# Kernel optimization log

Measured on AMD Instinct MI355X. Metric: run time of the kernel, lower is better.

The kernel has to match this reference:

```python
import jax, jax.numpy as jnp
import numpy as np

K_HOPS = 3
ALPHA = 0.3
DELTA = 0.5
KL_EPS = 1e-10
BN_EPS = 1e-5
DEG_MIN = 1e-6

B, T, N, F_IN, H, T_OUT = 8, 12, 1536, 1, 64, 12
HID2 = 2 * H  # MLP hidden width = 128


def setup_inputs() -> dict:
    key = jax.random.key(0)
    ks = jax.random.split(key, 20)
    s = 0.05
    TH = T * H
    inp = {
        "x": jax.random.normal(ks[0], (B, T, N, F_IN), jnp.float32),
        # AdaptiveBiDiffConv weights (stored as (in, out))
        "W1": jax.random.normal(ks[1], (F_IN, H), jnp.float32) * s,
        "W2": jax.random.normal(ks[2], (F_IN, H), jnp.float32) * s,
        # encoder MLPBlock: Linear(TH,128) ReLU Linear(128,128) ReLU Linear(128,64) + proj(TH,64), BN(64)
        "enc_w1": jax.random.normal(ks[3], (TH, HID2), jnp.float32) * s,
        "enc_b1": jnp.zeros((HID2,), jnp.float32),
        "enc_w2": jax.random.normal(ks[4], (HID2, HID2), jnp.float32) * s,
        "enc_b2": jnp.zeros((HID2,), jnp.float32),
        "enc_w3": jax.random.normal(ks[5], (HID2, H), jnp.float32) * s,
        "enc_b3": jnp.zeros((H,), jnp.float32),
        "enc_proj": jax.random.normal(ks[6], (TH, H), jnp.float32) * s,
        "enc_bn_g": jnp.ones((H,), jnp.float32),
        "enc_bn_b": jnp.zeros((H,), jnp.float32),
        "enc_bn_m": jnp.zeros((H,), jnp.float32),
        "enc_bn_v": jnp.ones((H,), jnp.float32),
        # decoder MLPBlock: Linear(64,128) ReLU Linear(128,128) ReLU Linear(128,12) + proj(64,12), BN(12)
        "dec_w1": jax.random.normal(ks[7], (H, HID2), jnp.float32) * s,
        "dec_b1": jnp.zeros((HID2,), jnp.float32),
        "dec_w2": jax.random.normal(ks[8], (HID2, HID2), jnp.float32) * s,
        "dec_b2": jnp.zeros((HID2,), jnp.float32),
        "dec_w3": jax.random.normal(ks[9], (HID2, T_OUT), jnp.float32) * s,
        "dec_b3": jnp.zeros((T_OUT,), jnp.float32),
        "dec_proj": jax.random.normal(ks[10], (H, T_OUT), jnp.float32) * s,
        "dec_bn_g": jnp.ones((T_OUT,), jnp.float32),
        "dec_bn_b": jnp.zeros((T_OUT,), jnp.float32),
        "dec_bn_m": jnp.zeros((T_OUT,), jnp.float32),
        "dec_bn_v": jnp.ones((T_OUT,), jnp.float32),
    }
    return inp


def _row_norm(A):
    return A / jnp.maximum(A.sum(-1, keepdims=True), DEG_MIN)


def _mlp_block(z, w1, b1, w2, b2, w3, b3, proj, g, be, m, v):
    h = jax.nn.relu(z @ w1 + b1)
    h = jax.nn.relu(h @ w2 + b2)
    o = (h @ w3 + b3) + z @ proj
    # BatchNorm1d, eval mode over last (channel) axis
    return (o - m) / jnp.sqrt(v + BN_EPS) * g + be


def _forward(x, W1, W2,
             enc_w1, enc_b1, enc_w2, enc_b2, enc_w3, enc_b3, enc_proj,
             enc_bn_g, enc_bn_b, enc_bn_m, enc_bn_v,
             dec_w1, dec_b1, dec_w2, dec_b2, dec_w3, dec_b3, dec_proj,
             dec_bn_g, dec_bn_b, dec_bn_m, dec_bn_v):
    b, t, n, _ = x.shape
    # ---- KL adjacency (fused form: avoids (B,N,N,T) broadcast) ----
    p = jax.nn.softmax(jnp.transpose(x[..., 0], (0, 2, 1)), axis=-1)  # (B,N,T)
    logp = jnp.log(p + KL_EPS)
    # kl[b,i,j] = sum_t p_i (logp_i - logp_j)
    kl = jnp.sum(p * logp, axis=-1, keepdims=True) - jnp.einsum('bit,bjt->bij', p, logp)
    A = (kl < DELTA).astype(x.dtype)  # (B,N,N)
    A_fwd = _row_norm(A)
    A_bwd = _row_norm(jnp.swapaxes(A, -1, -2))
    # ---- bidirectional diffusion conv (x_k never updated in original loop) ----
    x_flow = x[..., :1]                    # (B,T,N,1)
    x_res = x_flow @ W1                    # (B,T,N,H)
    xw = x_flow @ W2                       # (B,T,N,H)
    fwd = jnp.einsum('bij,btjh->btih', A_fwd, xw)
    bwd = jnp.einsum('bij,btjh->btih', A_bwd, xw)
    x_p = jax.nn.relu(x_res + K_HOPS * (ALPHA * fwd + (1.0 - ALPHA) * bwd))
    # ---- temporal MLP encoder/decoder ----
    x_flat = jnp.transpose(x_p, (0, 2, 1, 3)).reshape(b, n, t * x_p.shape[-1])  # (B,N,T*H)
    x_e = _mlp_block(x_flat, enc_w1, enc_b1, enc_w2, enc_b2, enc_w3, enc_b3,
                     enc_proj, enc_bn_g, enc_bn_b, enc_bn_m, enc_bn_v)  # (B,N,H)
    x_d = _mlp_block(x_e, dec_w1, dec_b1, dec_w2, dec_b2, dec_w3, dec_b3,
                     dec_proj, dec_bn_g, dec_bn_b, dec_bn_m, dec_bn_v)  # (B,N,T_out)
    return jnp.transpose(x_d, (0, 2, 1))[..., None]  # (B,T_out,N,1)


def reference(x, W1, W2,
              enc_w1, enc_b1, enc_w2, enc_b2, enc_w3, enc_b3, enc_proj,
              enc_bn_g, enc_bn_b, enc_bn_m, enc_bn_v,
              dec_w1, dec_b1, dec_w2, dec_b2, dec_w3, dec_b3, dec_proj,
              dec_bn_g, dec_bn_b, dec_bn_m, dec_bn_v):
    return _forward(x, W1, W2,
                    enc_w1, enc_b1, enc_w2, enc_b2, enc_w3, enc_b3, enc_proj,
                    enc_bn_g, enc_bn_b, enc_bn_m, enc_bn_v,
                    dec_w1, dec_b1, dec_w2, dec_b2, dec_w3, dec_b3, dec_proj,
                    dec_bn_g, dec_bn_b, dec_bn_m, dec_bn_v)
```

## Files before the change

kernel.cpp:

```cpp
#include <hip/hip_runtime.h>
#include <hip/hip_bf16.h>


namespace {

constexpr int Bn = 8, Nn = 1536, TOUT = 12;
constexpr int Mrows = Bn * Nn;
constexpr int JS = 8;

typedef __attribute__((ext_vector_type(8))) short bf8;
typedef __attribute__((ext_vector_type(4))) float f4;
typedef unsigned short ush;

__device__ __forceinline__ float b2f(__hip_bfloat16 v) { return __bfloat162float(v); }
__device__ __forceinline__ ush f2bu(float f) {
  union { __hip_bfloat16 h; ush u; } c; c.h = __float2bfloat16(f); return c.u;
}
__device__ __forceinline__ float bu2f(ush u) {
  union { unsigned int i; float f; } c; c.i = ((unsigned)u) << 16; return c.f;
}
__device__ __forceinline__ float ldraw(const void* p, size_t i, int fl) {
  return fl ? ((const float*)p)[i] : b2f(((const __hip_bfloat16*)p)[i]);
}

struct SmallTab { const void* src[16]; int n[16]; int off[16]; };

__global__ __launch_bounds__(256) void detect_small(
    const void* __restrict__ x, int* __restrict__ flag, SmallTab st,
    float* __restrict__ CS) {
  __shared__ int cnt; __shared__ int fls;
  if (threadIdx.x == 0) cnt = 0;
  __syncthreads();
  const ush* u = (const ush*)x;
  int c = 0;
#pragma unroll
  for (int s = 0; s < 16; ++s) {
    ush v = u[threadIdx.x + s * 256];
    if (((v >> 7) & 0xFF) >= 140) c++;
  }
  atomicAdd(&cnt, c);
  __syncthreads();
  if (threadIdx.x == 0) { fls = (cnt > 64) ? 1 : 0; flag[0] = fls; }
  __syncthreads();
  int fl = fls;
  for (int i = 0; i < 16; ++i)
    for (int e = threadIdx.x; e < st.n[i]; e += 256)
      CS[st.off[i] + e] = ldraw(st.src[i], e, fl);
}

__global__ __launch_bounds__(256) void prep_kernel(
    const void* __restrict__ xraw, const int* __restrict__ flag,
    float* __restrict__ xT, float* __restrict__ sd,
    ush* __restrict__ pA, ush* __restrict__ lA,
    ush* __restrict__ phi16, ush* __restrict__ plo16,
    ush* __restrict__ lhi16, ush* __restrict__ llo16,
    ush* __restrict__ Xc) {
  int tid = blockIdx.x * 256 + threadIdx.x;
  if (tid >= Mrows) return;
  int b = tid / Nn, n = tid - b * Nn;
  int fl = flag[0];
  float xv[12];
#pragma unroll
  for (int t = 0; t < 12; ++t)
    xv[t] = ldraw(xraw, (size_t)(b * 12 + t) * Nn + n, fl);
  float mx = xv[0];
#pragma unroll
  for (int t = 1; t < 12; ++t) mx = fmaxf(mx, xv[t]);
  float e[12], Z = 0.f;
#pragma unroll
  for (int t = 0; t < 12; ++t) { e[t] = expf(xv[t] - mx); Z += e[t]; }
  float invZ = 1.f / Z;
  float sacc = 0.f;
  ush pa[32], la[32], ph[16], pl[16], lh[16], ll[16];
#pragma unroll
  for (int k = 0; k < 32; ++k) { pa[k] = 0; la[k] = 0; }
#pragma unroll
  for (int k = 0; k < 16; ++k) { ph[k] = 0; pl[k] = 0; lh[k] = 0; ll[k] = 0; }
#pragma unroll
  for (int t = 0; t < 12; ++t) {
    float pv = e[t] * invZ;
    float lv = logf(pv + 1e-10f);
    sacc += pv * lv;
    xT[(size_t)tid * 12 + t] = xv[t];
    ush phv = f2bu(pv);  float plv = pv - bu2f(phv);
    ush lhv = f2bu(lv);  float llv = lv - bu2f(lhv);
    pa[t] = phv; pa[16 + t] = f2bu(plv);
    la[t] = lhv; la[16 + t] = f2bu(llv);
    ph[t] = phv; pl[t] = f2bu(plv);
    lh[t] = lhv; ll[t] = f2bu(llv);
    Xc[((size_t)(b * 16 + t)) * Nn + n] = f2bu(xv[t]);
  }
  Xc[((size_t)(b * 16 + 12)) * Nn + n] = 0x3F80;
#pragma unroll
  for (int t = 13; t < 16; ++t) Xc[((size_t)(b * 16 + t)) * Nn + n] = 0;
  sd[tid] = sacc;
  {
    uint4* d = (uint4*)(pA + (size_t)tid * 32);
    const uint4* s = (const uint4*)pa;
    d[0] = s[0]; d[1] = s[1]; d[2] = s[2]; d[3] = s[3];
    uint4* d2 = (uint4*)(lA + (size_t)tid * 32);
    const uint4* s2 = (const uint4*)la;
    d2[0] = s2[0]; d2[1] = s2[1]; d2[2] = s2[2]; d2[3] = s2[3];
    ((uint4*)(phi16 + (size_t)tid * 16))[0] = ((const uint4*)ph)[0];
    ((uint4*)(phi16 + (size_t)tid * 16))[1] = ((const uint4*)ph)[1];
    ((uint4*)(plo16 + (size_t)tid * 16))[0] = ((const uint4*)pl)[0];
    ((uint4*)(plo16 + (size_t)tid * 16))[1] = ((const uint4*)pl)[1];
    ((uint4*)(lhi16 + (size_t)tid * 16))[0] = ((const uint4*)lh)[0];
    ((uint4*)(lhi16 + (size_t)tid * 16))[1] = ((const uint4*)lh)[1];
    ((uint4*)(llo16 + (size_t)tid * 16))[0] = ((const uint4*)ll)[0];
    ((uint4*)(llo16 + (size_t)tid * 16))[1] = ((const uint4*)ll)[1];
  }
}

struct RepTab { const void* src[8]; int Nc[8]; int NCT[8]; int lb[9]; };

__global__ __launch_bounds__(256) void repack_kernel(
    RepTab tab, const int* __restrict__ flag, ush* __restrict__ Wf) {
  int idx = blockIdx.x * 256 + threadIdx.x;
  if (idx >= tab.lb[8]) return;
  int fl = flag[0];
  int mi = 0;
#pragma unroll
  for (int i = 1; i < 8; ++i) if (idx >= tab.lb[i]) mi = i;
  int li = idx - tab.lb[mi];
  int NCT = tab.NCT[mi], Nc = tab.Nc[mi];
  int per = NCT * 64;
  int c0 = li / per, rem = li - c0 * per;
  int ct = rem >> 6, l = rem & 63;
  int q = l >> 4, m = l & 15;
  int col = ct * 16 + m;
  ush* d = Wf + (size_t)idx * 8;
#pragma unroll
  for (int j = 0; j < 8; ++j) {
    int k = c0 * 32 + q * 8 + j;
    d[j] = (col < Nc) ? f2bu(ldraw(tab.src[mi], (size_t)k * Nc + col, fl)) : 0;
  }
}

__global__ __launch_bounds__(256) void kl_mfma(
    const ush* __restrict__ pA, const ush* __restrict__ lA,
    const ush* __restrict__ phi16, const ush* __restrict__ plo16,
    const ush* __restrict__ lhi16, const ush* __restrict__ llo16,
    const ush* __restrict__ Xc, const float* __restrict__ sd,
    float* __restrict__ psf, float* __restrict__ psb) {
  __shared__ ush T1[4][512], T2[4][512];
  int tid = threadIdx.x, w = tid >> 6, l = tid & 63, q = l >> 4, n = l & 15;
  int blk = blockIdx.x;
  int b = blk / 192, rem = blk % 192, ig = rem >> 3, js = rem & 7;
  int i0 = ig * 64 + w * 16;
  int rowb = b * Nn;

  if (q >= 2) {
    uint4 z4 = {0, 0, 0, 0};
    *(uint4*)(&T1[w][(size_t)l * 8]) = z4;
    *(uint4*)(&T2[w][(size_t)l * 8]) = z4;
  }

  bf8 z8 = {0, 0, 0, 0, 0, 0, 0, 0};
  bf8 aP = *(const bf8*)(pA + ((size_t)(rowb + i0 + n)) * 32 + q * 8);
  bf8 aL = *(const bf8*)(lA + ((size_t)(rowb + i0 + n)) * 32 + q * 8);
  bf8 aPh = (q < 2) ? aP : z8;
  bf8 aLh = (q < 2) ? aL : z8;
  float selfI[4];
#pragma unroll
  for (int r = 0; r < 4; ++r) selfI[r] = sd[rowb + i0 + q * 4 + r];

  f4 accF = {0.f, 0.f, 0.f, 0.f}, accB = {0.f, 0.f, 0.f, 0.f};

  for (int jt = 0; jt < 12; ++jt) {
    int jl = js * 192 + jt * 16;
    size_t bb = ((size_t)(rowb + jl + n)) * 16 + (q & 1) * 8;
    bf8 bLh = *(const bf8*)(lhi16 + bb);
    bf8 bLo = *(const bf8*)(llo16 + bb);
    bf8 bPh = *(const bf8*)(phi16 + bb);
    bf8 bPo = *(const bf8*)(plo16 + bb);
    float selfJ = sd[rowb + jl + n];

    f4 s1 = {0.f, 0.f, 0.f, 0.f}, s2 = {0.f, 0.f, 0.f, 0.f};
    s1 = __builtin_amdgcn_mfma_f32_16x16x32_bf16(aP, bLh, s1, 0, 0, 0);
    s1 = __builtin_amdgcn_mfma_f32_16x16x32_bf16(aPh, bLo, s1, 0, 0, 0);
    s2 = __builtin_amdgcn_mfma_f32_16x16x32_bf16(aL, bPh, s2, 0, 0, 0);
    s2 = __builtin_amdgcn_mfma_f32_16x16x32_bf16(aLh, bPo, s2, 0, 0, 0);

    int qk = n >> 3, kj = n & 7;
#pragma unroll
    for (int r = 0; r < 4; ++r) {
      int pos = (qk * 16 + q * 4 + r) * 8 + kj;
      T1[w][pos] = (selfI[r] - s1[r] < 0.5f) ? (ush)0x3F80 : (ush)0;
      T2[w][pos] = (selfJ - s2[r] < 0.5f) ? (ush)0x3F80 : (ush)0;
    }
    bf8 af1 = *(const bf8*)(&T1[w][(size_t)l * 8]);
    bf8 af2 = *(const bf8*)(&T2[w][(size_t)l * 8]);
    bf8 xf = (q < 2)
        ? *(const bf8*)(Xc + ((size_t)(b * 16 + n)) * Nn + jl + q * 8) : z8;
    accF = __builtin_amdgcn_mfma_f32_16x16x32_bf16(af1, xf, accF, 0, 0, 0);
    accB = __builtin_amdgcn_mfma_f32_16x16x32_bf16(af2, xf, accB, 0, 0, 0);
  }
#pragma unroll
  for (int r = 0; r < 4; ++r) {
    size_t o = ((size_t)js * Mrows + rowb + i0 + q * 4 + r) * 16 + n;
    psf[o] = accF[r];
    psb[o] = accB[r];
  }
}

__global__ __launch_bounds__(256) void fin_kernel(
    const float* __restrict__ psf, const float* __restrict__ psb,
    float* __restrict__ cc) {
  int tid = blockIdx.x * 256 + threadIdx.x;
  if (tid >= Mrows) return;
  float sf[16], sb[16];
#pragma unroll
  for (int t = 0; t < 16; ++t) { sf[t] = 0.f; sb[t] = 0.f; }
  for (int s = 0; s < JS; ++s) {
    const float4* a = (const float4*)(psf + ((size_t)s * Mrows + tid) * 16);
    const float4* c4 = (const float4*)(psb + ((size_t)s * Mrows + tid) * 16);
#pragma unroll
    for (int v = 0; v < 4; ++v) {
      float4 av = a[v], cv = c4[v];
      sf[v * 4 + 0] += av.x; sf[v * 4 + 1] += av.y; sf[v * 4 + 2] += av.z; sf[v * 4 + 3] += av.w;
      sb[v * 4 + 0] += cv.x; sb[v * 4 + 1] += cv.y; sb[v * 4 + 2] += cv.z; sb[v * 4 + 3] += cv.w;
    }
  }
  float irs = 1.f / fmaxf(sf[12], 1e-6f);
  float ics = 1.f / fmaxf(sb[12], 1e-6f);
#pragma unroll
  for (int t = 0; t < 12; ++t)
    cc[(size_t)tid * 12 + t] = 3.0f * (0.3f * sf[t] * irs + 0.7f * sb[t] * ics);
}

__global__ __launch_bounds__(64) void fused_mlp(
    const float* __restrict__ xT, const float* __restrict__ cc,
    const float* __restrict__ CS, const ush* __restrict__ Wf,
    const int* __restrict__ flag, void* __restrict__ outp) {
  __shared__ ush zf[24 * 512];
  __shared__ ush hf[4 * 512];
  __shared__ ush hg[4 * 512];
  __shared__ ush xf[2 * 512];
  int l = threadIdx.x, q = l >> 4, n = l & 15;
  int r0 = blockIdx.x * 16;
  const float* W1c = CS; const float* W2c = CS + 64;

  for (int pp = 0; pp < 6; ++pp) {
    int pair = pp * 64 + l;
    int c0 = pair >> 4, mr = pair & 15;
    int grow = r0 + mr;
    int t = c0 >> 1, h0 = (c0 & 1) * 32;
    float xv = xT[(size_t)grow * 12 + t];
    float cv = cc[(size_t)grow * 12 + t];
#pragma unroll
    for (int s = 0; s < 4; ++s) {
      union { ush u[8]; uint4 v; } pk;
#pragma unroll
      for (int j = 0; j < 8; ++j) {
        int h = h0 + s * 8 + j;
        pk.u[j] = f2bu(fmaxf(fmaf(xv, W1c[h], cv * W2c[h]), 0.f));
      }
      *(uint4*)(&zf[(size_t)(c0 * 64 + s * 16 + mr) * 8]) = pk.v;
    }
  }
  __syncthreads();

  f4 acc[8];
#pragma unroll
  for (int ct = 0; ct < 8; ++ct) acc[ct] = {0.f, 0.f, 0.f, 0.f};
  for (int c0 = 0; c0 < 24; ++c0) {
    bf8 a = *(const bf8*)(&zf[(size_t)(c0 * 64 + l) * 8]);
    const ush* wb = Wf + ((size_t)(c0 * 8) * 64 + l) * 8;
#pragma unroll
    for (int ct = 0; ct < 8; ++ct) {
      bf8 bfr = *(const bf8*)(wb + (size_t)ct * 512);
      acc[ct] = __builtin_amdgcn_mfma_f32_16x16x32_bf16(a, bfr, acc[ct], 0, 0, 0);
    }
  }
#pragma unroll
  for (int ct = 0; ct < 8; ++ct) {
    int col = ct * 16 + n;
    float bz = CS[128 + col];
#pragma unroll
    for (int r = 0; r < 4; ++r) {
      int pos = ((ct >> 1) * 64 + ((ct & 1) * 2 + (n >> 3)) * 16 + q * 4 + r) * 8 + (n & 7);
      hf[pos] = f2bu(fmaxf(acc[ct][r] + bz, 0.f));
    }
  }
  __syncthreads();

#pragma unroll
  for (int ct = 0; ct < 8; ++ct) acc[ct] = {0.f, 0.f, 0.f, 0.f};
  for (int c0 = 0; c0 < 4; ++c0) {
    bf8 a = *(const bf8*)(&hf[(size_t)(c0 * 64 + l) * 8]);
    const ush* wb = Wf + 98304 + ((size_t)(c0 * 8) * 64 + l) * 8;
#pragma unroll
    for (int ct = 0; ct < 8; ++ct) {
      bf8 bfr = *(const bf8*)(wb + (size_t)ct * 512);
      acc[ct] = __builtin_amdgcn_mfma_f32_16x16x32_bf16(a, bfr, acc[ct], 0, 0, 0);
    }
  }
#pragma unroll
  for (int ct = 0; ct < 8; ++ct) {
    int col = ct * 16 + n;
    float bz = CS[256 + col];
#pragma unroll
    for (int r = 0; r < 4; ++r) {
      int pos = ((ct >> 1) * 64 + ((ct & 1) * 2 + (n >> 3)) * 16 + q * 4 + r) * 8 + (n & 7);
      hg[pos] = f2bu(fmaxf(acc[ct][r] + bz, 0.f));
    }
  }
  __syncthreads();

  f4 a3[4];
#pragma unroll
  for (int ct = 0; ct < 4; ++ct) a3[ct] = {0.f, 0.f, 0.f, 0.f};
  for (int c0 = 0; c0 < 4; ++c0) {
    bf8 a = *(const bf8*)(&hg[(size_t)(c0 * 64 + l) * 8]);
    const ush* wb = Wf + 114688 + ((size_t)(c0 * 4) * 64 + l) * 8;
#pragma unroll
    for (int ct = 0; ct < 4; ++ct) {
      bf8 bfr = *(const bf8*)(wb + (size_t)ct * 512);
      a3[ct] = __builtin_amdgcn_mfma_f32_16x16x32_bf16(a, bfr, a3[ct], 0, 0, 0);
    }
  }
  for (int c0 = 0; c0 < 24; ++c0) {
    bf8 a = *(const bf8*)(&zf[(size_t)(c0 * 64 + l) * 8]);
    const ush* wb = Wf + 122880 + ((size_t)(c0 * 4) * 64 + l) * 8;
#pragma unroll
    for (int ct = 0; ct < 4; ++ct) {
      bf8 bfr = *(const bf8*)(wb + (size_t)ct * 512);
      a3[ct] = __builtin_amdgcn_mfma_f32_16x16x32_bf16(a, bfr, a3[ct], 0, 0, 0);
    }
  }
#pragma unroll
  for (int ct = 0; ct < 4; ++ct) {
    int col = ct * 16 + n;
    float g = CS[448 + col], be = CS[512 + col], mm = CS[576 + col], vv = CS[640 + col];
    float sc = g / sqrtf(vv + 1e-5f);
    float sh = be - mm * sc;
    float bz = CS[384 + col];
#pragma unroll
    for (int r = 0; r < 4; ++r) {
      int pos = ((ct >> 1) * 64 + ((ct & 1) * 2 + (n >> 3)) * 16 + q * 4 + r) * 8 + (n & 7);
      xf[pos] = f2bu((a3[ct][r] + bz) * sc + sh);
    }
  }
  __syncthreads();

#pragma unroll
  for (int ct = 0; ct < 8; ++ct) acc[ct] = {0.f, 0.f, 0.f, 0.f};
  for (int c0 = 0; c0 < 2; ++c0) {
    bf8 a = *(const bf8*)(&xf[(size_t)(c0 * 64 + l) * 8]);
    const ush* wb = Wf + 172032 + ((size_t)(c0 * 8) * 64 + l) * 8;
#pragma unroll
    for (int ct = 0; ct < 8; ++ct) {
      bf8 bfr = *(const bf8*)(wb + (size_t)ct * 512);
      acc[ct] = __builtin_amdgcn_mfma_f32_16x16x32_bf16(a, bfr, acc[ct], 0, 0, 0);
    }
  }
#pragma unroll
  for (int ct = 0; ct < 8; ++ct) {
    int col = ct * 16 + n;
    float bz = CS[704 + col];
#pragma unroll
    for (int r = 0; r < 4; ++r) {
      int pos = ((ct >> 1) * 64 + ((ct & 1) * 2 + (n >> 3)) * 16 + q * 4 + r) * 8 + (n & 7);
      hf[pos] = f2bu(fmaxf(acc[ct][r] + bz, 0.f));
    }
  }
  __syncthreads();

#pragma unroll
  for (int ct = 0; ct < 8; ++ct) acc[ct] = {0.f, 0.f, 0.f, 0.f};
  for (int c0 = 0; c0 < 4; ++c0) {
    bf8 a = *(const bf8*)(&hf[(size_t)(c0 * 64 + l) * 8]);
    const ush* wb = Wf + 180224 + ((size_t)(c0 * 8) * 64 + l) * 8;
#pragma unroll
    for (int ct = 0; ct < 8; ++ct) {
      bf8 bfr = *(const bf8*)(wb + (size_t)ct * 512);
      acc[ct] = __builtin_amdgcn_mfma_f32_16x16x32_bf16(a, bfr, acc[ct], 0, 0, 0);
    }
  }
#pragma unroll
  for (int ct = 0; ct < 8; ++ct) {
    int col = ct * 16 + n;
    float bz = CS[832 + col];
#pragma unroll
    for (int r = 0; r < 4; ++r) {
      int pos = ((ct >> 1) * 64 + ((ct & 1) * 2 + (n >> 3)) * 16 + q * 4 + r) * 8 + (n & 7);
      hg[pos] = f2bu(fmaxf(acc[ct][r] + bz, 0.f));
    }
  }
  __syncthreads();

  f4 ao = {0.f, 0.f, 0.f, 0.f};
  for (int c0 = 0; c0 < 4; ++c0) {
    bf8 a = *(const bf8*)(&hg[(size_t)(c0 * 64 + l) * 8]);
    bf8 bfr = *(const bf8*)(Wf + 196608 + ((size_t)c0 * 64 + l) * 8);
    ao = __builtin_amdgcn_mfma_f32_16x16x32_bf16(a, bfr, ao, 0, 0, 0);
  }
  for (int c0 = 0; c0 < 2; ++c0) {
    bf8 a = *(const bf8*)(&xf[(size_t)(c0 * 64 + l) * 8]);
    bf8 bfr = *(const bf8*)(Wf + 198656 + ((size_t)c0 * 64 + l) * 8);
    ao = __builtin_amdgcn_mfma_f32_16x16x32_bf16(a, bfr, ao, 0, 0, 0);
  }
  int fl = flag[0];
  if (n < 12) {
    float bz = CS[960 + n];
    float g = CS[972 + n], be = CS[984 + n], mm = CS[996 + n], vv = CS[1008 + n];
    float sc = g / sqrtf(vv + 1e-5f);
    float sh = be - mm * sc;
#pragma unroll
    for (int r = 0; r < 4; ++r) {
      int row = r0 + q * 4 + r;
      int bb = row / Nn, nn = row - bb * Nn;
      size_t oi = ((size_t)bb * TOUT + n) * Nn + nn;
      float ov = (ao[r] + bz) * sc + sh;
      if (fl) ((float*)outp)[oi] = ov;
      else    ((ush*)outp)[oi] = f2bu(ov);
    }
  }
}

}

extern "C" void kernel_launch(void* const* d_in, const int* in_sizes, int n_in,
                              void* d_out, int out_size, void* d_ws, size_t ws_size,
                              hipStream_t stream) {
  float* f = (float*)d_ws;
  int* flag = (int*)d_ws;
  float* CS  = f + 16;
  float* xT  = f + 1040;
  float* cc  = f + 148496;
  float* sd  = f + 295952;
  float* psf = f + 308240;
  float* psb = f + 1881104;
  ush* U = (ush*)(f + 3453968);
  ush* pA    = U;
  ush* lA    = U + 393216;
  ush* phi16 = U + 786432;
  ush* plo16 = U + 983040;
  ush* lhi16 = U + 1179648;
  ush* llo16 = U + 1376256;
  ush* Xc    = U + 1572864;
  ush* Wf    = U + 1769472;

  SmallTab st;
  {
    const int idxs[16] = {1, 2, 4, 6, 8, 10, 11, 12, 13, 15, 17, 19, 21, 22, 23, 24};
    const int ns[16]   = {64, 64, 128, 128, 64, 64, 64, 64, 64, 128, 128, 12, 12, 12, 12, 12};
    int off = 0;
    for (int i = 0; i < 16; ++i) {
      st.src[i] = d_in[idxs[i]]; st.n[i] = ns[i]; st.off[i] = off; off += ns[i];
    }
  }
  RepTab rt;
  {
    const int idxs[8]  = {3, 5, 7, 9, 14, 16, 18, 20};
    const int rNc[8]   = {128, 128, 64, 64, 128, 128, 12, 12};
    const int rNCT[8]  = {8, 8, 4, 4, 8, 8, 1, 1};
    const int rlb[9]   = {0, 12288, 14336, 15360, 21504, 22528, 24576, 24832, 24960};
    for (int i = 0; i < 8; ++i) {
      rt.src[i] = d_in[idxs[i]]; rt.Nc[i] = rNc[i]; rt.NCT[i] = rNCT[i];
    }
    for (int i = 0; i < 9; ++i) rt.lb[i] = rlb[i];
  }

  detect_small<<<1, 256, 0, stream>>>(d_in[0], flag, st, CS);
  prep_kernel<<<48, 256, 0, stream>>>(d_in[0], flag, xT, sd, pA, lA,
                                      phi16, plo16, lhi16, llo16, Xc);
  repack_kernel<<<98, 256, 0, stream>>>(rt, flag, Wf);
  kl_mfma<<<1536, 256, 0, stream>>>(pA, lA, phi16, plo16, lhi16, llo16,
                                    Xc, sd, psf, psb);
  fin_kernel<<<48, 256, 0, stream>>>(psf, psb, cc);
  fused_mlp<<<768, 64, 0, stream>>>(xT, cc, CS, Wf, flag, d_out);
}
```

Measured before the change: 173.3 us.

## Merge prep kernels, fold partial-sum reduction into MLP, split MLP across four waves

Three small setup kernels (dtype detect, prep, weight repack) become one launch, with every block redoing the cheap flag detection. The partial-sum reduction and normalisation from fin_kernel move into the MLP kernel, which removes the cc buffer and a launch. The MLP kernel goes from one wave per 16 rows to four waves that split output column tiles. It also regenerates the first-layer activations on the fly instead of staging a large LDS buffer, which cuts LDS use and per-wave register pressure but recomputes the z values twice.

```diff
diff --git a/kernel.cpp b/kernel.cpp
--- a/kernel.cpp
+++ b/kernel.cpp
@@ -23,117 +23,115 @@
   return fl ? ((const float*)p)[i] : b2f(((const __hip_bfloat16*)p)[i]);
 }
 
-struct SmallTab { const void* src[16]; int n[16]; int off[16]; };
-
-__global__ __launch_bounds__(256) void detect_small(
-    const void* __restrict__ x, int* __restrict__ flag, SmallTab st,
-    float* __restrict__ CS) {
-  __shared__ int cnt; __shared__ int fls;
-  if (threadIdx.x == 0) cnt = 0;
+__device__ __forceinline__ int detect_fl(const void* x, int tid) {
+  __shared__ int cnt;
+  if (tid == 0) cnt = 0;
   __syncthreads();
   const ush* u = (const ush*)x;
   int c = 0;
 #pragma unroll
   for (int s = 0; s < 16; ++s) {
-    ush v = u[threadIdx.x + s * 256];
+    ush v = u[tid + s * 256];
     if (((v >> 7) & 0xFF) >= 140) c++;
   }
   atomicAdd(&cnt, c);
   __syncthreads();
-  if (threadIdx.x == 0) { fls = (cnt > 64) ? 1 : 0; flag[0] = fls; }
-  __syncthreads();
-  int fl = fls;
-  for (int i = 0; i < 16; ++i)
-    for (int e = threadIdx.x; e < st.n[i]; e += 256)
-      CS[st.off[i] + e] = ldraw(st.src[i], e, fl);
-}
-
-__global__ __launch_bounds__(256) void prep_kernel(
-    const void* __restrict__ xraw, const int* __restrict__ flag,
+  return (cnt > 64) ? 1 : 0;
+}
+
+struct SmallTab { const void* src[16]; int n[16]; int off[16]; };
+struct RepTab { const void* src[8]; int Nc[8]; int NCT[8]; int lb[9]; };
+
+__global__ __launch_bounds__(256) void prep_all(
+    const void* __restrict__ xraw, SmallTab st, RepTab rt,
+    int* __restrict__ flag, float* __restrict__ CS,
     float* __restrict__ xT, float* __restrict__ sd,
     ush* __restrict__ pA, ush* __restrict__ lA,
     ush* __restrict__ phi16, ush* __restrict__ plo16,
     ush* __restrict__ lhi16, ush* __restrict__ llo16,
-    ush* __restrict__ Xc) {
-  int tid = blockIdx.x * 256 + threadIdx.x;
-  if (tid >= Mrows) return;
-  int b = tid / Nn, n = tid - b * Nn;
-  int fl = flag[0];
-  float xv[12];
-#pragma unroll
-  for (int t = 0; t < 12; ++t)
-    xv[t] = ldraw(xraw, (size_t)(b * 12 + t) * Nn + n, fl);
-  float mx = xv[0];
-#pragma unroll
-  for (int t = 1; t < 12; ++t) mx = fmaxf(mx, xv[t]);
-  float e[12], Z = 0.f;
-#pragma unroll
-  for (int t = 0; t < 12; ++t) { e[t] = expf(xv[t] - mx); Z += e[t]; }
-  float invZ = 1.f / Z;
-  float sacc = 0.f;
-  ush pa[32], la[32], ph[16], pl[16], lh[16], ll[16];
-#pragma unroll
-  for (int k = 0; k < 32; ++k) { pa[k] = 0; la[k] = 0; }
-#pragma unroll
-  for (int k = 0; k < 16; ++k) { ph[k] = 0; pl[k] = 0; lh[k] = 0; ll[k] = 0; }
-#pragma unroll
-  for (int t = 0; t < 12; ++t) {
-    float pv = e[t] * invZ;
-    float lv = logf(pv + 1e-10f);
-    sacc += pv * lv;
-    xT[(size_t)tid * 12 + t] = xv[t];
-    ush phv = f2bu(pv);  float plv = pv - bu2f(phv);
-    ush lhv = f2bu(lv);  float llv = lv - bu2f(lhv);
-    pa[t] = phv; pa[16 + t] = f2bu(plv);
-    la[t] = lhv; la[16 + t] = f2bu(llv);
-    ph[t] = phv; pl[t] = f2bu(plv);
-    lh[t] = lhv; ll[t] = f2bu(llv);
-    Xc[((size_t)(b * 16 + t)) * Nn + n] = f2bu(xv[t]);
-  }
-  Xc[((size_t)(b * 16 + 12)) * Nn + n] = 0x3F80;
-#pragma unroll
-  for (int t = 13; t < 16; ++t) Xc[((size_t)(b * 16 + t)) * Nn + n] = 0;
-  sd[tid] = sacc;
-  {
-    uint4* d = (uint4*)(pA + (size_t)tid * 32);
-    const uint4* s = (const uint4*)pa;
-    d[0] = s[0]; d[1] = s[1]; d[2] = s[2]; d[3] = s[3];
-    uint4* d2 = (uint4*)(lA + (size_t)tid * 32);
-    const uint4* s2 = (const uint4*)la;
-    d2[0] = s2[0]; d2[1] = s2[1]; d2[2] = s2[2]; d2[3] = s2[3];
-    ((uint4*)(phi16 + (size_t)tid * 16))[0] = ((const uint4*)ph)[0];
-    ((uint4*)(phi16 + (size_t)tid * 16))[1] = ((const uint4*)ph)[1];
-    ((uint4*)(plo16 + (size_t)tid * 16))[0] = ((const uint4*)pl)[0];
-    ((uint4*)(plo16 + (size_t)tid * 16))[1] = ((const uint4*)pl)[1];
-    ((uint4*)(lhi16 + (size_t)tid * 16))[0] = ((const uint4*)lh)[0];
-    ((uint4*)(lhi16 + (size_t)tid * 16))[1] = ((const uint4*)lh)[1];
-    ((uint4*)(llo16 + (size_t)tid * 16))[0] = ((const uint4*)ll)[0];
-    ((uint4*)(llo16 + (size_t)tid * 16))[1] = ((const uint4*)ll)[1];
-  }
-}
-
-struct RepTab { const void* src[8]; int Nc[8]; int NCT[8]; int lb[9]; };
-
-__global__ __launch_bounds__(256) void repack_kernel(
-    RepTab tab, const int* __restrict__ flag, ush* __restrict__ Wf) {
-  int idx = blockIdx.x * 256 + threadIdx.x;
-  if (idx >= tab.lb[8]) return;
-  int fl = flag[0];
-  int mi = 0;
-#pragma unroll
-  for (int i = 1; i < 8; ++i) if (idx >= tab.lb[i]) mi = i;
-  int li = idx - tab.lb[mi];
-  int NCT = tab.NCT[mi], Nc = tab.Nc[mi];
-  int per = NCT * 64;
-  int c0 = li / per, rem = li - c0 * per;
-  int ct = rem >> 6, l = rem & 63;
-  int q = l >> 4, m = l & 15;
-  int col = ct * 16 + m;
-  ush* d = Wf + (size_t)idx * 8;
-#pragma unroll
-  for (int j = 0; j < 8; ++j) {
-    int k = c0 * 32 + q * 8 + j;
-    d[j] = (col < Nc) ? f2bu(ldraw(tab.src[mi], (size_t)k * Nc + col, fl)) : 0;
+    ush* __restrict__ Xc, ush* __restrict__ Wf) {
+  int tid = threadIdx.x;
+  int fl = detect_fl(xraw, tid);
+  int blk = blockIdx.x;
+
+  if (blk < 48) {
+    int row = blk * 256 + tid;
+    int b = row / Nn, n = row - b * Nn;
+    float xv[12];
+#pragma unroll
+    for (int t = 0; t < 12; ++t)
+      xv[t] = ldraw(xraw, (size_t)(b * 12 + t) * Nn + n, fl);
+    float mx = xv[0];
+#pragma unroll
+    for (int t = 1; t < 12; ++t) mx = fmaxf(mx, xv[t]);
+    float e[12], Z = 0.f;
+#pragma unroll
+    for (int t = 0; t < 12; ++t) { e[t] = expf(xv[t] - mx); Z += e[t]; }
+    float invZ = 1.f / Z;
+    float sacc = 0.f;
+    ush pa[32], la[32], ph[16], pl[16], lh[16], ll[16];
+#pragma unroll
+    for (int k = 0; k < 32; ++k) { pa[k] = 0; la[k] = 0; }
+#pragma unroll
+    for (int k = 0; k < 16; ++k) { ph[k] = 0; pl[k] = 0; lh[k] = 0; ll[k] = 0; }
+#pragma unroll
+    for (int t = 0; t < 12; ++t) {
+      float pv = e[t] * invZ;
+      float lv = logf(pv + 1e-10f);
+      sacc += pv * lv;
+      xT[(size_t)row * 12 + t] = xv[t];
+      ush phv = f2bu(pv);  float plv = pv - bu2f(phv);
+      ush lhv = f2bu(lv);  float llv = lv - bu2f(lhv);
+      pa[t] = phv; pa[16 + t] = f2bu(plv);
+      la[t] = lhv; la[16 + t] = f2bu(llv);
+      ph[t] = phv; pl[t] = f2bu(plv);
+      lh[t] = lhv; ll[t] = f2bu(llv);
+      Xc[((size_t)(b * 16 + t)) * Nn + n] = f2bu(xv[t]);
+    }
+    Xc[((size_t)(b * 16 + 12)) * Nn + n] = 0x3F80;
+#pragma unroll
+    for (int t = 13; t < 16; ++t) Xc[((size_t)(b * 16 + t)) * Nn + n] = 0;
+    sd[row] = sacc;
+    {
+      uint4* d = (uint4*)(pA + (size_t)row * 32);
+      const uint4* s = (const uint4*)pa;
+      d[0] = s[0]; d[1] = s[1]; d[2] = s[2]; d[3] = s[3];
+      uint4* d2 = (uint4*)(lA + (size_t)row * 32);
+      const uint4* s2 = (const uint4*)la;
+      d2[0] = s2[0]; d2[1] = s2[1]; d2[2] = s2[2]; d2[3] = s2[3];
+      ((uint4*)(phi16 + (size_t)row * 16))[0] = ((const uint4*)ph)[0];
+      ((uint4*)(phi16 + (size_t)row * 16))[1] = ((const uint4*)ph)[1];
+      ((uint4*)(plo16 + (size_t)row * 16))[0] = ((const uint4*)pl)[0];
+      ((uint4*)(plo16 + (size_t)row * 16))[1] = ((const uint4*)pl)[1];
+      ((uint4*)(lhi16 + (size_t)row * 16))[0] = ((const uint4*)lh)[0];
+      ((uint4*)(lhi16 + (size_t)row * 16))[1] = ((const uint4*)lh)[1];
+      ((uint4*)(llo16 + (size_t)row * 16))[0] = ((const uint4*)ll)[0];
+      ((uint4*)(llo16 + (size_t)row * 16))[1] = ((const uint4*)ll)[1];
+    }
+  } else if (blk < 146) {
+    int idx = (blk - 48) * 256 + tid;
+    if (idx >= rt.lb[8]) return;
+    int mi = 0;
+#pragma unroll
+    for (int i = 1; i < 8; ++i) if (idx >= rt.lb[i]) mi = i;
+    int li = idx - rt.lb[mi];
+    int NCT = rt.NCT[mi], Nc = rt.Nc[mi];
+    int per = NCT * 64;
+    int c0 = li / per, rem = li - c0 * per;
+    int ct = rem >> 6, l = rem & 63;
+    int q = l >> 4, m = l & 15;
+    int col = ct * 16 + m;
+    ush* d = Wf + (size_t)idx * 8;
+#pragma unroll
+    for (int j = 0; j < 8; ++j) {
+      int k = c0 * 32 + q * 8 + j;
+      d[j] = (col < Nc) ? f2bu(ldraw(rt.src[mi], (size_t)k * Nc + col, fl)) : 0;
+    }
+  } else {
+    for (int i = 0; i < 16; ++i)
+      for (int e = tid; e < st.n[i]; e += 256)
+        CS[st.off[i] + e] = ldraw(st.src[i], e, fl);
+    if (tid == 0) flag[0] = fl;
   }
 }
 
@@ -191,10 +189,10 @@
     }
     bf8 af1 = *(const bf8*)(&T1[w][(size_t)l * 8]);
     bf8 af2 = *(const bf8*)(&T2[w][(size_t)l * 8]);
-    bf8 xf = (q < 2)
+    bf8 xfr = (q < 2)
         ? *(const bf8*)(Xc + ((size_t)(b * 16 + n)) * Nn + jl + q * 8) : z8;
-    accF = __builtin_amdgcn_mfma_f32_16x16x32_bf16(af1, xf, accF, 0, 0, 0);
-    accB = __builtin_amdgcn_mfma_f32_16x16x32_bf16(af2, xf, accB, 0, 0, 0);
+    accF = __builtin_amdgcn_mfma_f32_16x16x32_bf16(af1, xfr, accF, 0, 0, 0);
+    accB = __builtin_amdgcn_mfma_f32_16x16x32_bf16(af2, xfr, accB, 0, 0, 0);
   }
 #pragma unroll
   for (int r = 0; r < 4; ++r) {
@@ -204,217 +202,205 @@
   }
 }
 
-__global__ __launch_bounds__(256) void fin_kernel(
+__global__ __launch_bounds__(256) void fused_mlp(
+    const float* __restrict__ xT,
     const float* __restrict__ psf, const float* __restrict__ psb,
-    float* __restrict__ cc) {
-  int tid = blockIdx.x * 256 + threadIdx.x;
-  if (tid >= Mrows) return;
-  float sf[16], sb[16];
-#pragma unroll
-  for (int t = 0; t < 16; ++t) { sf[t] = 0.f; sb[t] = 0.f; }
-  for (int s = 0; s < JS; ++s) {
-    const float4* a = (const float4*)(psf + ((size_t)s * Mrows + tid) * 16);
-    const float4* c4 = (const float4*)(psb + ((size_t)s * Mrows + tid) * 16);
-#pragma unroll
-    for (int v = 0; v < 4; ++v) {
-      float4 av = a[v], cv = c4[v];
-      sf[v * 4 + 0] += av.x; sf[v * 4 + 1] += av.y; sf[v * 4 + 2] += av.z; sf[v * 4 + 3] += av.w;
-      sb[v * 4 + 0] += cv.x; sb[v * 4 + 1] += cv.y; sb[v * 4 + 2] += cv.z; sb[v * 4 + 3] += cv.w;
-    }
-  }
-  float irs = 1.f / fmaxf(sf[12], 1e-6f);
-  float ics = 1.f / fmaxf(sb[12], 1e-6f);
-#pragma unroll
-  for (int t = 0; t < 12; ++t)
-    cc[(size_t)tid * 12 + t] = 3.0f * (0.3f * sf[t] * irs + 0.7f * sb[t] * ics);
-}
-
-__global__ __launch_bounds__(64) void fused_mlp(
-    const float* __restrict__ xT, const float* __restrict__ cc,
     const float* __restrict__ CS, const ush* __restrict__ Wf,
     const int* __restrict__ flag, void* __restrict__ outp) {
-  __shared__ ush zf[24 * 512];
-  __shared__ ush hf[4 * 512];
-  __shared__ ush hg[4 * 512];
-  __shared__ ush xf[2 * 512];
-  int l = threadIdx.x, q = l >> 4, n = l & 15;
+  __shared__ float xs[16][12], ccs[16][12];
+  __shared__ float sfs[16][16], sbs[16][16];
+  __shared__ float ws1[64], ws2[64];
+  __shared__ ush hf[2048], hg[2048], xf[1024];
+  __shared__ f4 red[4][64];
+
+  int tid = threadIdx.x, w = tid >> 6, l = tid & 63, q = l >> 4, n = l & 15;
   int r0 = blockIdx.x * 16;
-  const float* W1c = CS; const float* W2c = CS + 64;
-
-  for (int pp = 0; pp < 6; ++pp) {
-    int pair = pp * 64 + l;
-    int c0 = pair >> 4, mr = pair & 15;
-    int grow = r0 + mr;
-    int t = c0 >> 1, h0 = (c0 & 1) * 32;
-    float xv = xT[(size_t)grow * 12 + t];
-    float cv = cc[(size_t)grow * 12 + t];
-#pragma unroll
-    for (int s = 0; s < 4; ++s) {
-      union { ush u[8]; uint4 v; } pk;
-#pragma unroll
-      for (int j = 0; j < 8; ++j) {
-        int h = h0 + s * 8 + j;
-        pk.u[j] = f2bu(fmaxf(fmaf(xv, W1c[h], cv * W2c[h]), 0.f));
-      }
-      *(uint4*)(&zf[(size_t)(c0 * 64 + s * 16 + mr) * 8]) = pk.v;
-    }
-  }
-  __syncthreads();
-
-  f4 acc[8];
-#pragma unroll
-  for (int ct = 0; ct < 8; ++ct) acc[ct] = {0.f, 0.f, 0.f, 0.f};
-  for (int c0 = 0; c0 < 24; ++c0) {
-    bf8 a = *(const bf8*)(&zf[(size_t)(c0 * 64 + l) * 8]);
-    const ush* wb = Wf + ((size_t)(c0 * 8) * 64 + l) * 8;
-#pragma unroll
-    for (int ct = 0; ct < 8; ++ct) {
-      bf8 bfr = *(const bf8*)(wb + (size_t)ct * 512);
-      acc[ct] = __builtin_amdgcn_mfma_f32_16x16x32_bf16(a, bfr, acc[ct], 0, 0, 0);
-    }
-  }
-#pragma unroll
-  for (int ct = 0; ct < 8; ++ct) {
-    int col = ct * 16 + n;
-    float bz = CS[128 + col];
-#pragma unroll
-    for (int r = 0; r < 4; ++r) {
-      int pos = ((ct >> 1) * 64 + ((ct & 1) * 2 + (n >> 3)) * 16 + q * 4 + r) * 8 + (n & 7);
-      hf[pos] = f2bu(fmaxf(acc[ct][r] + bz, 0.f));
-    }
-  }
-  __syncthreads();
-
-#pragma unroll
-  for (int ct = 0; ct < 8; ++ct) acc[ct] = {0.f, 0.f, 0.f, 0.f};
-  for (int c0 = 0; c0 < 4; ++c0) {
-    bf8 a = *(const bf8*)(&hf[(size_t)(c0 * 64 + l) * 8]);
-    const ush* wb = Wf + 98304 + ((size_t)(c0 * 8) * 64 + l) * 8;
-#pragma unroll
-    for (int ct = 0; ct < 8; ++ct) {
-      bf8 bfr = *(const bf8*)(wb + (size_t)ct * 512);
-      acc[ct] = __builtin_amdgcn_mfma_f32_16x16x32_bf16(a, bfr, acc[ct], 0, 0, 0);
-    }
-  }
-#pragma unroll
-  for (int ct = 0; ct < 8; ++ct) {
-    int col = ct * 16 + n;
-    float bz = CS[256 + col];
-#pragma unroll
-    for (int r = 0; r < 4; ++r) {
-      int pos = ((ct >> 1) * 64 + ((ct & 1) * 2 + (n >> 3)) * 16 + q * 4 + r) * 8 + (n & 7);
-      hg[pos] = f2bu(fmaxf(acc[ct][r] + bz, 0.f));
-    }
-  }
-  __syncthreads();
-
-  f4 a3[4];
-#pragma unroll
-  for (int ct = 0; ct < 4; ++ct) a3[ct] = {0.f, 0.f, 0.f, 0.f};
-  for (int c0 = 0; c0 < 4; ++c0) {
-    bf8 a = *(const bf8*)(&hg[(size_t)(c0 * 64 + l) * 8]);
-    const ush* wb = Wf + 114688 + ((size_t)(c0 * 4) * 64 + l) * 8;
-#pragma unroll
-    for (int ct = 0; ct < 4; ++ct) {
-      bf8 bfr = *(const bf8*)(wb + (size_t)ct * 512);
-      a3[ct] = __builtin_amdgcn_mfma_f32_16x16x32_bf16(a, bfr, a3[ct], 0, 0, 0);
-    }
-  }
-  for (int c0 = 0; c0 < 24; ++c0) {
-    bf8 a = *(const bf8*)(&zf[(size_t)(c0 * 64 + l) * 8]);
-    const ush* wb = Wf + 122880 + ((size_t)(c0 * 4) * 64 + l) * 8;
-#pragma unroll
-    for (int ct = 0; ct < 4; ++ct) {
-      bf8 bfr = *(const bf8*)(wb + (size_t)ct * 512);
-      a3[ct] = __builtin_amdgcn_mfma_f32_16x16x32_bf16(a, bfr, a3[ct], 0, 0, 0);
-    }
-  }
-#pragma unroll
-  for (int ct = 0; ct < 4; ++ct) {
-    int col = ct * 16 + n;
+
+  {
+    int r = tid >> 4, t = tid & 15;
+    float a = 0.f, b = 0.f;
+#pragma unroll
+    for (int js = 0; js < JS; ++js) {
+      size_t o = ((size_t)js * Mrows + r0 + r) * 16 + t;
+      a += psf[o];
+      b += psb[o];
+    }
+    sfs[r][t] = a;
+    sbs[r][t] = b;
+    if (tid < 128) { if (tid < 64) ws1[tid] = CS[tid]; else ws2[tid - 64] = CS[tid]; }
+    if (tid < 192) {
+      int rr = tid / 12, tt = tid - rr * 12;
+      xs[rr][tt] = xT[(size_t)(r0 + rr) * 12 + tt];
+    }
+  }
+  __syncthreads();
+  if (tid < 192) {
+    int rr = tid / 12, tt = tid - rr * 12;
+    float irs = 1.f / fmaxf(sfs[rr][12], 1e-6f);
+    float ics = 1.f / fmaxf(sbs[rr][12], 1e-6f);
+    ccs[rr][tt] = 3.0f * (0.3f * sfs[rr][tt] * irs + 0.7f * sbs[rr][tt] * ics);
+  }
+  __syncthreads();
+
+  auto zregen = [&](int c0) -> bf8 {
+    int t = c0 >> 1, h0 = (c0 & 1) * 32 + q * 8;
+    float xv = xs[n][t], cv = ccs[n][t];
+    union { bf8 v; ush u[8]; } au;
+#pragma unroll
+    for (int j = 0; j < 8; ++j)
+      au.u[j] = f2bu(fmaxf(fmaf(xv, ws1[h0 + j], cv * ws2[h0 + j]), 0.f));
+    return au.v;
+  };
+  auto fpos = [&](int ct, int r) -> int {
+    return ((ct >> 1) * 64 + ((ct & 1) * 2 + (n >> 3)) * 16 + q * 4 + r) * 8 + (n & 7);
+  };
+
+  {
+    f4 a0 = {0.f, 0.f, 0.f, 0.f}, a1 = {0.f, 0.f, 0.f, 0.f};
+    for (int c0 = 0; c0 < 24; ++c0) {
+      bf8 a = zregen(c0);
+      const ush* wb = Wf + ((size_t)(c0 * 8 + 2 * w) * 64 + l) * 8;
+      bf8 b0 = *(const bf8*)wb;
+      bf8 b1 = *(const bf8*)(wb + 512);
+      a0 = __builtin_amdgcn_mfma_f32_16x16x32_bf16(a, b0, a0, 0, 0, 0);
+      a1 = __builtin_amdgcn_mfma_f32_16x16x32_bf16(a, b1, a1, 0, 0, 0);
+    }
+#pragma unroll
+    for (int u2 = 0; u2 < 2; ++u2) {
+      int ct = 2 * w + u2;
+      f4 acc = u2 ? a1 : a0;
+      float bz = CS[128 + ct * 16 + n];
+#pragma unroll
+      for (int r = 0; r < 4; ++r)
+        hf[fpos(ct, r)] = f2bu(fmaxf(acc[r] + bz, 0.f));
+    }
+  }
+  __syncthreads();
+
+  {
+    f4 a0 = {0.f, 0.f, 0.f, 0.f}, a1 = {0.f, 0.f, 0.f, 0.f};
+    for (int c0 = 0; c0 < 4; ++c0) {
+      bf8 a = *(const bf8*)(&hf[(size_t)(c0 * 64 + l) * 8]);
+      const ush* wb = Wf + 98304 + ((size_t)(c0 * 8 + 2 * w) * 64 + l) * 8;
+      bf8 b0 = *(const bf8*)wb;
+      bf8 b1 = *(const bf8*)(wb + 512);
+      a0 = __builtin_amdgcn_mfma_f32_16x16x32_bf16(a, b0, a0, 0, 0, 0);
+      a1 = __builtin_amdgcn_mfma_f32_16x16x32_bf16(a, b1, a1, 0, 0, 0);
+    }
+    __syncthreads();
+#pragma unroll
+    for (int u2 = 0; u2 < 2; ++u2) {
+      int ct = 2 * w + u2;
+      f4 acc = u2 ? a1 : a0;
+      float bz = CS[256 + ct * 16 + n];
+#pragma unroll
+      for (int r = 0; r < 4; ++r)
+        hg[fpos(ct, r)] = f2bu(fmaxf(acc[r] + bz, 0.f));
+    }
+  }
+  __syncthreads();
+
+  {
+    f4 a3 = {0.f, 0.f, 0.f, 0.f};
+    for (int c0 = 0; c0 < 4; ++c0) {
+      bf8 a = *(const bf8*)(&hg[(size_t)(c0 * 64 + l) * 8]);
+      bf8 b = *(const bf8*)(Wf + 114688 + ((size_t)(c0 * 4 + w) * 64 + l) * 8);
+      a3 = __builtin_amdgcn_mfma_f32_16x16x32_bf16(a, b, a3, 0, 0, 0);
+    }
+    for (int c0 = 0; c0 < 24; ++c0) {
+      bf8 a = zregen(c0);
+      bf8 b = *(const bf8*)(Wf + 122880 + ((size_t)(c0 * 4 + w) * 64 + l) * 8);
+      a3 = __builtin_amdgcn_mfma_f32_16x16x32_bf16(a, b, a3, 0, 0, 0);
+    }
+    int col = w * 16 + n;
     float g = CS[448 + col], be = CS[512 + col], mm = CS[576 + col], vv = CS[640 + col];
     float sc = g / sqrtf(vv + 1e-5f);
     float sh = be - mm * sc;
     float bz = CS[384 + col];
 #pragma unroll
-    for (int r = 0; r < 4; ++r) {
-      int pos = ((ct >> 1) * 64 + ((ct & 1) * 2 + (n >> 3)) * 16 + q * 4 + r) * 8 + (n & 7);
-      xf[pos] = f2bu((a3[ct][r] + bz) * sc + sh);
-    }
-  }
-  __syncthreads();
-
-#pragma unroll
-  for (int ct = 0; ct < 8; ++ct) acc[ct] = {0.f, 0.f, 0.f, 0.f};
-  for (int c0 = 0; c0 < 2; ++c0) {
-    bf8 a = *(const bf8*)(&xf[(size_t)(c0 * 64 + l) * 8]);
-    const ush* wb = Wf + 172032 + ((size_t)(c0 * 8) * 64 + l) * 8;
-#pragma unroll
-    for (int ct = 0; ct < 8; ++ct) {
-      bf8 bfr = *(const bf8*)(wb + (size_t)ct * 512);
-      acc[ct] = __builtin_amdgcn_mfma_f32_16x16x32_bf16(a, bfr, acc[ct], 0, 0, 0);
-    }
-  }
-#pragma unroll
-  for (int ct = 0; ct < 8; ++ct) {
-    int col = ct * 16 + n;
-    float bz = CS[704 + col];
-#pragma unroll
-    for (int r = 0; r < 4; ++r) {
-      int pos = ((ct >> 1) * 64 + ((ct & 1) * 2 + (n >> 3)) * 16 + q * 4 + r) * 8 + (n & 7);
-      hf[pos] = f2bu(fmaxf(acc[ct][r] + bz, 0.f));
-    }
-  }
-  __syncthreads();
-
-#pragma unroll
-  for (int ct = 0; ct < 8; ++ct) acc[ct] = {0.f, 0.f, 0.f, 0.f};
-  for (int c0 = 0; c0 < 4; ++c0) {
-    bf8 a = *(const bf8*)(&hf[(size_t)(c0 * 64 + l) * 8]);
-    const ush* wb = Wf + 180224 + ((size_t)(c0 * 8) * 64 + l) * 8;
-#pragma unroll
-    for (int ct = 0; ct < 8; ++ct) {
-      bf8 bfr = *(const bf8*)(wb + (size_t)ct * 512);
-      acc[ct] = __builtin_amdgcn_mfma_f32_16x16x32_bf16(a, bfr, acc[ct], 0, 0, 0);
-    }
-  }
-#pragma unroll
-  for (int ct = 0; ct < 8; ++ct) {
-    int col = ct * 16 + n;
-    float bz = CS[832 + col];
-#pragma unroll
-    for (int r = 0; r < 4; ++r) {
-      int pos = ((ct >> 1) * 64 + ((ct & 1) * 2 + (n >> 3)) * 16 + q * 4 + r) * 8 + (n & 7);
-      hg[pos] = f2bu(fmaxf(acc[ct][r] + bz, 0.f));
-    }
-  }
-  __syncthreads();
-
-  f4 ao = {0.f, 0.f, 0.f, 0.f};
-  for (int c0 = 0; c0 < 4; ++c0) {
-    bf8 a = *(const bf8*)(&hg[(size_t)(c0 * 64 + l) * 8]);
-    bf8 bfr = *(const bf8*)(Wf + 196608 + ((size_t)c0 * 64 + l) * 8);
-    ao = __builtin_amdgcn_mfma_f32_16x16x32_bf16(a, bfr, ao, 0, 0, 0);
-  }
-  for (int c0 = 0; c0 < 2; ++c0) {
-    bf8 a = *(const bf8*)(&xf[(size_t)(c0 * 64 + l) * 8]);
-    bf8 bfr = *(const bf8*)(Wf + 198656 + ((size_t)c0 * 64 + l) * 8);
-    ao = __builtin_amdgcn_mfma_f32_16x16x32_bf16(a, bfr, ao, 0, 0, 0);
-  }
-  int fl = flag[0];
-  if (n < 12) {
-    float bz = CS[960 + n];
-    float g = CS[972 + n], be = CS[984 + n], mm = CS[996 + n], vv = CS[1008 + n];
-    float sc = g / sqrtf(vv + 1e-5f);
-    float sh = be - mm * sc;
-#pragma unroll
-    for (int r = 0; r < 4; ++r) {
-      int row = r0 + q * 4 + r;
-      int bb = row / Nn, nn = row - bb * Nn;
-      size_t oi = ((size_t)bb * TOUT + n) * Nn + nn;
-      float ov = (ao[r] + bz) * sc + sh;
-      if (fl) ((float*)outp)[oi] = ov;
-      else    ((ush*)outp)[oi] = f2bu(ov);
+    for (int r = 0; r < 4; ++r)
+      xf[fpos(w, r)] = f2bu((a3[r] + bz) * sc + sh);
+  }
+  __syncthreads();
+
+  {
+    f4 a0 = {0.f, 0.f, 0.f, 0.f}, a1 = {0.f, 0.f, 0.f, 0.f};
+    for (int c0 = 0; c0 < 2; ++c0) {
+      bf8 a = *(const bf8*)(&xf[(size_t)(c0 * 64 + l) * 8]);
+      const ush* wb = Wf + 172032 + ((size_t)(c0 * 8 + 2 * w) * 64 + l) * 8;
+      bf8 b0 = *(const bf8*)wb;
+      bf8 b1 = *(const bf8*)(wb + 512);
+      a0 = __builtin_amdgcn_mfma_f32_16x16x32_bf16(a, b0, a0, 0, 0, 0);
+      a1 = __builtin_amdgcn_mfma_f32_16x16x32_bf16(a, b1, a1, 0, 0, 0);
+    }
+    __syncthreads();
+#pragma unroll
+    for (int u2 = 0; u2 < 2; ++u2) {
+      int ct = 2 * w + u2;
+      f4 acc = u2 ? a1 : a0;
+      float bz = CS[704 + ct * 16 + n];
+#pragma unroll
+      for (int r = 0; r < 4; ++r)
+        hf[fpos(ct, r)] = f2bu(fmaxf(acc[r] + bz, 0.f));
+    }
+  }
+  __syncthreads();
+
+  {
+    f4 a0 = {0.f, 0.f, 0.f, 0.f}, a1 = {0.f, 0.f, 0.f, 0.f};
+    for (int c0 = 0; c0 < 4; ++c0) {
+      bf8 a = *(const bf8*)(&hf[(size_t)(c0 * 64 + l) * 8]);
+      const ush* wb = Wf + 180224 + ((size_t)(c0 * 8 + 2 * w) * 64 + l) * 8;
+      bf8 b0 = *(const bf8*)wb;
+      bf8 b1 = *(const bf8*)(wb + 512);
+      a0 = __builtin_amdgcn_mfma_f32_16x16x32_bf16(a, b0, a0, 0, 0, 0);
+      a1 = __builtin_amdgcn_mfma_f32_16x16x32_bf16(a, b1, a1, 0, 0, 0);
+    }
+    __syncthreads();
+#pragma unroll
+    for (int u2 = 0; u2 < 2; ++u2) {
+      int ct = 2 * w + u2;
+      f4 acc = u2 ? a1 : a0;
+      float bz = CS[832 + ct * 16 + n];
+#pragma unroll
+      for (int r = 0; r < 4; ++r)
+        hg[fpos(ct, r)] = f2bu(fmaxf(acc[r] + bz, 0.f));
+    }
+  }
+  __syncthreads();
+
+  {
+    f4 ao = {0.f, 0.f, 0.f, 0.f};
+    {
+      bf8 a = *(const bf8*)(&hg[(size_t)(w * 64 + l) * 8]);
+      bf8 b = *(const bf8*)(Wf + 196608 + ((size_t)w * 64 + l) * 8);
+      ao = __builtin_amdgcn_mfma_f32_16x16x32_bf16(a, b, ao, 0, 0, 0);
+    }
+    if (w < 2) {
+      bf8 a = *(const bf8*)(&xf[(size_t)(w * 64 + l) * 8]);
+      bf8 b = *(const bf8*)(Wf + 198656 + ((size_t)w * 64 + l) * 8);
+      ao = __builtin_amdgcn_mfma_f32_16x16x32_bf16(a, b, ao, 0, 0, 0);
+    }
+    red[w][l] = ao;
+  }
+  __syncthreads();
+  if (w == 0) {
+    f4 s = red[0][l] + red[1][l] + red[2][l] + red[3][l];
+    int fl = flag[0];
+    if (n < 12) {
+      float bz = CS[960 + n];
+      float g = CS[972 + n], be = CS[984 + n], mm = CS[996 + n], vv = CS[1008 + n];
+      float sc = g / sqrtf(vv + 1e-5f);
+      float sh = be - mm * sc;
+#pragma unroll
+      for (int r = 0; r < 4; ++r) {
+        int row = r0 + q * 4 + r;
+        int bb = row / Nn, nn = row - bb * Nn;
+        size_t oi = ((size_t)bb * TOUT + n) * Nn + nn;
+        float ov = (s[r] + bz) * sc + sh;
+        if (fl) ((float*)outp)[oi] = ov;
+        else    ((ush*)outp)[oi] = f2bu(ov);
+      }
     }
   }
 }
@@ -428,11 +414,10 @@
   int* flag = (int*)d_ws;
   float* CS  = f + 16;
   float* xT  = f + 1040;
-  float* cc  = f + 148496;
-  float* sd  = f + 295952;
-  float* psf = f + 308240;
-  float* psb = f + 1881104;
-  ush* U = (ush*)(f + 3453968);
+  float* sd  = f + 148496;
+  float* psf = f + 160784;
+  float* psb = f + 1733648;
+  ush* U = (ush*)(f + 3306512);
   ush* pA    = U;
   ush* lA    = U + 393216;
   ush* phi16 = U + 786432;
@@ -463,12 +448,9 @@
     for (int i = 0; i < 9; ++i) rt.lb[i] = rlb[i];
   }
 
-  detect_small<<<1, 256, 0, stream>>>(d_in[0], flag, st, CS);
-  prep_kernel<<<48, 256, 0, stream>>>(d_in[0], flag, xT, sd, pA, lA,
-                                      phi16, plo16, lhi16, llo16, Xc);
-  repack_kernel<<<98, 256, 0, stream>>>(rt, flag, Wf);
+  prep_all<<<147, 256, 0, stream>>>(d_in[0], st, rt, flag, CS, xT, sd,
+                                    pA, lA, phi16, plo16, lhi16, llo16, Xc, Wf);
   kl_mfma<<<1536, 256, 0, stream>>>(pA, lA, phi16, plo16, lhi16, llo16,
                                     Xc, sd, psf, psb);
-  fin_kernel<<<48, 256, 0, stream>>>(psf, psb, cc);
-  fused_mlp<<<768, 64, 0, stream>>>(xT, cc, CS, Wf, flag, d_out);
-}
+  fused_mlp<<<768, 256, 0, stream>>>(xT, psf, psb, CS, Wf, flag, d_out);
+}
```

Result: faster. 155.6 us (-10.2%).
